# Optimization experiments

Hardware: AMD Instinct MI355X
Metric: run time of the kernel (lower is better)

Reference implementation:

```python
import jax, jax.numpy as jnp
import numpy as np

TOP_K = 2


def setup_inputs() -> dict:
    key = jax.random.key(0)
    k1, k2, k3, k4, k5 = jax.random.split(key, 5)
    B, S, D, E, F = 2, 1024, 2048, 8, 768
    scale_in = 1.0 / np.sqrt(D)
    scale_ff = 1.0 / np.sqrt(F)
    return {
        "x": jax.random.normal(k1, (B, S, D), dtype=jnp.float32),
        "w_gate_router": jax.random.normal(k2, (E, D), dtype=jnp.float32) * scale_in,
        "w_gate_proj": jax.random.normal(k3, (E, F, D), dtype=jnp.float32) * scale_in,
        "w_up_proj": jax.random.normal(k4, (E, F, D), dtype=jnp.float32) * scale_in,
        "w_down_proj": jax.random.normal(k5, (E, D, F), dtype=jnp.float32) * scale_ff,
    }


def moe_forward(x, w_gate_router, w_gate_proj, w_up_proj, w_down_proj):
    E = w_gate_router.shape[0]
    # Router: scores [B,S,E], top-k selection, softmax over the k selected scores.
    scores = jnp.einsum("bsd,ed->bse", x, w_gate_router)
    topk_scores, topk_idx = jax.lax.top_k(scores, TOP_K)          # [B,S,K]
    topk_probs = jax.nn.softmax(topk_scores, axis=-1)             # [B,S,K]
    # Dense combine weights: zero for unselected experts (== scatter of topk_probs).
    weights = jnp.sum(topk_probs[..., None] * jax.nn.one_hot(topk_idx, E, dtype=x.dtype), axis=-2)  # [B,S,E]
    # Per-expert SwiGLU computed densely over all tokens (same math as
    # gather/dispatch-per-expert followed by scatter-add combine).
    gate = jnp.einsum("bsd,efd->bsef", x, w_gate_proj)            # [B,S,E,F]
    up = jnp.einsum("bsd,efd->bsef", x, w_up_proj)
    hidden = jax.nn.silu(gate) * up                                # [B,S,E,F]
    # Weighted combine: sum_e weights[b,s,e] * (hidden @ w_down[e].T)
    out = jnp.einsum("bsef,edf,bse->bsd", hidden, w_down_proj, weights)
    return out


def reference(x, w_gate_router, w_gate_proj, w_up_proj, w_down_proj):
    return moe_forward(x, w_gate_router, w_gate_proj, w_up_proj, w_down_proj)
```

## Files before the change

### kernel.cpp

```cpp
#include <hip/hip_runtime.h>

#define T_TOK 2048
#define DIM   2048
#define NEXP  8
#define FF    768
#define NGRP  16

typedef unsigned short u16;
typedef unsigned int   u32;
typedef __bf16 bf16x8 __attribute__((ext_vector_type(8)));
typedef float  f32x4  __attribute__((ext_vector_type(4)));
typedef u16    u16x4  __attribute__((ext_vector_type(4)));

#define AS1 __attribute__((address_space(1)))
#define AS3 __attribute__((address_space(3)))

__device__ __forceinline__ u16 f2bf(float f) {
    union { u32 i; float f; } v; v.f = f;
    u32 r = v.i + 0x7FFF + ((v.i >> 16) & 1);
    return (u16)(r >> 16);
}

__device__ __forceinline__ void gload16(const u16* g, u16* l) {
    __builtin_amdgcn_global_load_lds((const AS1 u32*)g, (AS3 u32*)l, 16, 0, 0);
}

__global__ void cvt_kernel(const float* __restrict__ s, u16* __restrict__ d, int n4) {
    int i = blockIdx.x * blockDim.x + threadIdx.x;
    int st = gridDim.x * blockDim.x;
    for (; i < n4; i += st) {
        f32x4 v = ((const f32x4*)s)[i];
        u16x4 o;
#pragma unroll
        for (int j = 0; j < 4; j++) o[j] = f2bf(v[j]);
        ((u16x4*)d)[i] = o;
    }
}

__global__ void router_kernel(const float* __restrict__ x, const float* __restrict__ wr,
                              int* cnt, int* rt_e, float* rt_p) {
    int t = blockIdx.x;
    int lane = threadIdx.x;
    float xv[32];
#pragma unroll
    for (int i = 0; i < 32; i++) xv[i] = x[(size_t)t * DIM + i * 64 + lane];
    float s[NEXP];
#pragma unroll
    for (int e = 0; e < NEXP; e++) {
        float acc = 0.f;
#pragma unroll
        for (int i = 0; i < 32; i++) acc += xv[i] * wr[(size_t)e * DIM + i * 64 + lane];
        for (int off = 32; off; off >>= 1) acc += __shfl_xor(acc, off);
        s[e] = acc;
    }
    if (lane == 0) {
        int bi = 0; float bv = s[0];
        for (int e = 1; e < NEXP; e++) if (s[e] > bv) { bv = s[e]; bi = e; }
        float sv = -1e30f; int si = 0;
        for (int e = 0; e < NEXP; e++) { if (e == bi) continue; if (s[e] > sv) { sv = s[e]; si = e; } }
        float p0 = 1.f / (1.f + __expf(sv - bv));
        float p1 = 1.f - p0;
        rt_e[t * 2 + 0] = bi; rt_e[t * 2 + 1] = si;
        rt_p[t * 2 + 0] = p0; rt_p[t * 2 + 1] = p1;
        atomicAdd(&cnt[bi * 2 + 0], 1);
        atomicAdd(&cnt[si * 2 + 1], 1);
    }
}

__global__ void scan_kernel(const int* cnt, int* base, int* tile_g, int* tile_m0, int* ntiles) {
    if (threadIdx.x == 0 && blockIdx.x == 0) {
        int off = 0, nt = 0;
        for (int g = 0; g < NGRP; g++) {
            base[g] = off;
            int c = cnt[g];
            for (int m0 = 0; m0 < c; m0 += 128) { tile_g[nt] = g; tile_m0[nt] = m0; nt++; }
            off += c;
        }
        *ntiles = nt;
    }
}

__global__ void assign_kernel(const int* rt_e, const float* rt_p, const int* base,
                              int* poscnt, int* rowtok, float* rowprob) {
    int t = blockIdx.x * blockDim.x + threadIdx.x;
    if (t >= T_TOK) return;
    for (int k = 0; k < 2; k++) {
        int g = rt_e[t * 2 + k] * 2 + k;
        int pos = atomicAdd(&poscnt[g], 1);
        int row = base[g] + pos;
        rowtok[row] = t;
        rowprob[row] = rt_p[t * 2 + k];
    }
}

__launch_bounds__(256)
__global__ void gateup_kernel(const u16* __restrict__ xb, const u16* __restrict__ wgb,
                              const u16* __restrict__ wub,
                              const int* cnt, const int* base, const int* tile_g,
                              const int* tile_m0, const int* ntiles,
                              const int* rowtok, const float* rowprob,
                              u16* __restrict__ hidden) {
    int tile = blockIdx.x;
    if (tile >= *ntiles) return;
    int g = tile_g[tile], m0 = tile_m0[tile];
    int e = g >> 1;
    int f0 = blockIdx.y * 64;
    int cg = cnt[g], bg_ = base[g];

    __shared__ u16 As[128 * 32];
    __shared__ u16 Bs[128 * 32];
    __shared__ int   tks[128];
    __shared__ float ps[128];

    int tid = threadIdx.x;
    if (tid < 128) {
        int valid = (m0 + tid) < cg;
        tks[tid] = valid ? rowtok[bg_ + m0 + tid] : 0;
        ps[tid]  = valid ? rowprob[bg_ + m0 + tid] : 0.f;
    }
    __syncthreads();

    int wave = tid >> 6, lane = tid & 63;
    int quad = lane >> 4, l16 = lane & 15;
    int wr = wave >> 1, wc = wave & 1;

    int r4   = lane >> 2;
    int koff = (lane & 3) * 8;
    int arow0 = wave * 32 + r4;
    const u16* ga0 = xb + (size_t)tks[arow0] * DIM + koff;
    const u16* ga1 = xb + (size_t)tks[arow0 + 16] * DIM + koff;
    int c0 = wave * 2;
    const u16* wsrc0 = (c0 & 1) ? wub : wgb;
    const u16* wsrc1 = ((c0 + 1) & 1) ? wub : wgb;
    const u16* gb0 = wsrc0 + ((size_t)e * FF + f0 + ((c0) >> 1) * 16 + r4) * DIM + koff;
    const u16* gb1 = wsrc1 + ((size_t)e * FF + f0 + ((c0 + 1) >> 1) * 16 + r4) * DIM + koff;
    u16* lA0 = &As[(wave * 32) * 32];
    u16* lA1 = &As[(wave * 32 + 16) * 32];
    u16* lB0 = &Bs[(c0 * 16) * 32];
    u16* lB1 = &Bs[((c0 + 1) * 16) * 32];

    f32x4 acc[4][4] = {};

    for (int kk = 0; kk < DIM; kk += 32) {
        gload16(ga0 + kk, lA0);
        gload16(ga1 + kk, lA1);
        gload16(gb0 + kk, lB0);
        gload16(gb1 + kk, lB1);
        __syncthreads();
        bf16x8 a[4], b[4];
#pragma unroll
        for (int mi = 0; mi < 4; mi++)
            a[mi] = *(const bf16x8*)&As[(wr * 64 + mi * 16 + l16) * 32 + quad * 8];
#pragma unroll
        for (int ni = 0; ni < 4; ni++)
            b[ni] = *(const bf16x8*)&Bs[(wc * 64 + ni * 16 + l16) * 32 + quad * 8];
#pragma unroll
        for (int mi = 0; mi < 4; mi++)
#pragma unroll
            for (int ni = 0; ni < 4; ni++)
                acc[mi][ni] = __builtin_amdgcn_mfma_f32_16x16x32_bf16(a[mi], b[ni], acc[mi][ni], 0, 0, 0);
        __syncthreads();
    }

#pragma unroll
    for (int mi = 0; mi < 4; mi++) {
#pragma unroll
        for (int p = 0; p < 2; p++) {
            int f = f0 + (wc * 2 + p) * 16 + l16;
#pragma unroll
            for (int r = 0; r < 4; r++) {
                int m = wr * 64 + mi * 16 + quad * 4 + r;
                if (m0 + m < cg) {
                    float gv = acc[mi][p * 2][r], uv = acc[mi][p * 2 + 1][r];
                    float h = (gv / (1.f + __expf(-gv))) * uv * ps[m];
                    hidden[(size_t)(bg_ + m0 + m) * FF + f] = f2bf(h);
                }
            }
        }
    }
}

__launch_bounds__(256)
__global__ void down_kernel(const u16* __restrict__ hid, const u16* __restrict__ wdb,
                            const int* cnt, const int* base, const int* tile_g,
                            const int* tile_m0, const int* ntiles, const int* rowtok,
                            float* __restrict__ out) {
    int tile = blockIdx.x;
    if (tile >= *ntiles) return;
    int g = tile_g[tile], m0 = tile_m0[tile];
    int e = g >> 1;
    int d0 = blockIdx.y * 128;
    int cg = cnt[g], bg_ = base[g];

    __shared__ u16 As[128 * 32];
    __shared__ u16 Bs[128 * 32];
    __shared__ int tks[128];

    int tid = threadIdx.x;
    if (tid < 128) tks[tid] = ((m0 + tid) < cg) ? rowtok[bg_ + m0 + tid] : 0;
    __syncthreads();

    int wave = tid >> 6, lane = tid & 63;
    int quad = lane >> 4, l16 = lane & 15;
    int wr = wave >> 1, wc = wave & 1;

    int r4   = lane >> 2;
    int koff = (lane & 3) * 8;
    int arow0 = wave * 32 + r4;
    const u16* ga0 = hid + (size_t)(bg_ + m0 + arow0) * FF + koff;
    const u16* ga1 = hid + (size_t)(bg_ + m0 + arow0 + 16) * FF + koff;
    int c0 = wave * 2;
    const u16* gb0 = wdb + ((size_t)e * DIM + d0 + c0 * 16 + r4) * FF + koff;
    const u16* gb1 = wdb + ((size_t)e * DIM + d0 + (c0 + 1) * 16 + r4) * FF + koff;
    u16* lA0 = &As[(wave * 32) * 32];
    u16* lA1 = &As[(wave * 32 + 16) * 32];
    u16* lB0 = &Bs[(c0 * 16) * 32];
    u16* lB1 = &Bs[((c0 + 1) * 16) * 32];

    f32x4 acc[4][4] = {};

    for (int kk = 0; kk < FF; kk += 32) {
        gload16(ga0 + kk, lA0);
        gload16(ga1 + kk, lA1);
        gload16(gb0 + kk, lB0);
        gload16(gb1 + kk, lB1);
        __syncthreads();
        bf16x8 a[4], b[4];
#pragma unroll
        for (int mi = 0; mi < 4; mi++)
            a[mi] = *(const bf16x8*)&As[(wr * 64 + mi * 16 + l16) * 32 + quad * 8];
#pragma unroll
        for (int ni = 0; ni < 4; ni++)
            b[ni] = *(const bf16x8*)&Bs[(wc * 64 + ni * 16 + l16) * 32 + quad * 8];
#pragma unroll
        for (int mi = 0; mi < 4; mi++)
#pragma unroll
            for (int ni = 0; ni < 4; ni++)
                acc[mi][ni] = __builtin_amdgcn_mfma_f32_16x16x32_bf16(a[mi], b[ni], acc[mi][ni], 0, 0, 0);
        __syncthreads();
    }

#pragma unroll
    for (int mi = 0; mi < 4; mi++) {
#pragma unroll
        for (int ni = 0; ni < 4; ni++) {
            int d = d0 + wc * 64 + ni * 16 + l16;
#pragma unroll
            for (int r = 0; r < 4; r++) {
                int m = wr * 64 + mi * 16 + quad * 4 + r;
                if (m0 + m < cg) {
                    atomicAdd(&out[(size_t)tks[m] * DIM + d], acc[mi][ni][r]);
                }
            }
        }
    }
}

extern "C" void kernel_launch(void* const* d_in, const int* in_sizes, int n_in,
                              void* d_out, int out_size, void* d_ws, size_t ws_size,
                              hipStream_t stream) {
    const float* x  = (const float*)d_in[0];
    const float* wr = (const float*)d_in[1];
    const float* wg = (const float*)d_in[2];
    const float* wu = (const float*)d_in[3];
    const float* wd = (const float*)d_in[4];
    float* out = (float*)d_out;

    char* W = (char*)d_ws;
    int*   cnt     = (int*)(W + 0);
    int*   poscnt  = (int*)(W + 64);
    int*   base    = (int*)(W + 128);
    int*   ntiles  = (int*)(W + 192);
    int*   tile_g  = (int*)(W + 256);
    int*   tile_m0 = (int*)(W + 512);
    int*   rt_e    = (int*)(W + 1024);
    float* rt_p    = (float*)(W + 20480);
    int*   rowtok  = (int*)(W + 40960);
    float* rowprob = (float*)(W + 61440);
    u16*   hidden  = (u16*)(W + 81920);
    u16*   xb      = (u16*)(W + ((size_t)8  << 20));
    u16*   wgb     = (u16*)(W + ((size_t)17 << 20));
    u16*   wub     = (u16*)(W + ((size_t)43 << 20));
    u16*   wdb     = (u16*)(W + ((size_t)69 << 20));

    hipMemsetAsync(W, 0, 256, stream);
    hipMemsetAsync(d_out, 0, (size_t)out_size * 4, stream);

    const int NW = NEXP * FF * DIM / 4;
    const int NX = T_TOK * DIM / 4;
    cvt_kernel<<<1280, 256, 0, stream>>>(x,  xb,  NX);
    cvt_kernel<<<1280, 256, 0, stream>>>(wg, wgb, NW);
    cvt_kernel<<<1280, 256, 0, stream>>>(wu, wub, NW);
    cvt_kernel<<<1280, 256, 0, stream>>>(wd, wdb, NW);

    router_kernel<<<T_TOK, 64, 0, stream>>>(x, wr, cnt, rt_e, rt_p);
    scan_kernel<<<1, 64, 0, stream>>>(cnt, base, tile_g, tile_m0, ntiles);
    assign_kernel<<<8, 256, 0, stream>>>(rt_e, rt_p, base, poscnt, rowtok, rowprob);

    gateup_kernel<<<dim3(48, 12), 256, 0, stream>>>(xb, wgb, wub, cnt, base, tile_g, tile_m0,
                                                    ntiles, rowtok, rowprob, hidden);
    down_kernel<<<dim3(48, 16), 256, 0, stream>>>(hidden, wdb, cnt, base, tile_g, tile_m0,
                                                  ntiles, rowtok, out);
}
```

Baseline: 394.0 us.

## Merge weight conversions, double K-tile depth, replace atomics with per-slot bf16 combine

The four fp32-to-bf16 conversion launches become one kernel indexed by grid y. Both GEMM kernels now load 64-wide K tiles into LDS, halving the number of barrier pairs per K sweep. The down projection stops doing fp32 atomicAdd into a zeroed output: each top-k slot writes its own bf16 buffer, reusing the wgb region after gate/up finishes, and a final combine kernel adds the two buffers into fp32. This drops the output memset and the atomic traffic, but rounds partial results to bf16 and assumes each token appears exactly once per slot.

```diff
diff --git a/kernel.cpp b/kernel.cpp
--- a/kernel.cpp
+++ b/kernel.cpp
@@ -11,6 +11,7 @@
 typedef __bf16 bf16x8 __attribute__((ext_vector_type(8)));
 typedef float  f32x4  __attribute__((ext_vector_type(4)));
 typedef u16    u16x4  __attribute__((ext_vector_type(4)));
+typedef u16    u16x8  __attribute__((ext_vector_type(8)));
 
 #define AS1 __attribute__((address_space(1)))
 #define AS3 __attribute__((address_space(3)))
@@ -20,12 +21,25 @@
     u32 r = v.i + 0x7FFF + ((v.i >> 16) & 1);
     return (u16)(r >> 16);
 }
+__device__ __forceinline__ float bf2f(u16 u) {
+    union { u32 i; float f; } v; v.i = ((u32)u) << 16; return v.f;
+}
 
 __device__ __forceinline__ void gload16(const u16* g, u16* l) {
     __builtin_amdgcn_global_load_lds((const AS1 u32*)g, (AS3 u32*)l, 16, 0, 0);
 }
 
-__global__ void cvt_kernel(const float* __restrict__ s, u16* __restrict__ d, int n4) {
+__global__ void cvt4_kernel(const float* __restrict__ s0, u16* __restrict__ d0, int n0,
+                            const float* __restrict__ s1, u16* __restrict__ d1, int n1,
+                            const float* __restrict__ s2, u16* __restrict__ d2, int n2,
+                            const float* __restrict__ s3, u16* __restrict__ d3, int n3) {
+    const float* s; u16* d; int n4;
+    switch (blockIdx.y) {
+        case 0: s = s0; d = d0; n4 = n0; break;
+        case 1: s = s1; d = d1; n4 = n1; break;
+        case 2: s = s2; d = d2; n4 = n2; break;
+        default: s = s3; d = d3; n4 = n3; break;
+    }
     int i = blockIdx.x * blockDim.x + threadIdx.x;
     int st = gridDim.x * blockDim.x;
     for (; i < n4; i += st) {
@@ -107,8 +121,8 @@
     int f0 = blockIdx.y * 64;
     int cg = cnt[g], bg_ = base[g];
 
-    __shared__ u16 As[128 * 32];
-    __shared__ u16 Bs[128 * 32];
+    __shared__ u16 As[128 * 64];
+    __shared__ u16 Bs[128 * 64];
     __shared__ int   tks[128];
     __shared__ float ps[128];
 
@@ -124,41 +138,45 @@
     int quad = lane >> 4, l16 = lane & 15;
     int wr = wave >> 1, wc = wave & 1;
 
-    int r4   = lane >> 2;
-    int koff = (lane & 3) * 8;
-    int arow0 = wave * 32 + r4;
-    const u16* ga0 = xb + (size_t)tks[arow0] * DIM + koff;
-    const u16* ga1 = xb + (size_t)tks[arow0 + 16] * DIM + koff;
-    int c0 = wave * 2;
-    const u16* wsrc0 = (c0 & 1) ? wub : wgb;
-    const u16* wsrc1 = ((c0 + 1) & 1) ? wub : wgb;
-    const u16* gb0 = wsrc0 + ((size_t)e * FF + f0 + ((c0) >> 1) * 16 + r4) * DIM + koff;
-    const u16* gb1 = wsrc1 + ((size_t)e * FF + f0 + ((c0 + 1) >> 1) * 16 + r4) * DIM + koff;
-    u16* lA0 = &As[(wave * 32) * 32];
-    u16* lA1 = &As[(wave * 32 + 16) * 32];
-    u16* lB0 = &Bs[(c0 * 16) * 32];
-    u16* lB1 = &Bs[((c0 + 1) * 16) * 32];
+    int r8   = lane >> 3;
+    int koff = (lane & 7) * 8;
+    const u16* ga[4]; const u16* gb[4];
+    u16 *lA[4], *lB[4];
+#pragma unroll
+    for (int j = 0; j < 4; j++) {
+        int arow = wave * 32 + j * 8 + r8;
+        ga[j] = xb + (size_t)tks[arow] * DIM + koff;
+        lA[j] = &As[(wave * 32 + j * 8) * 64];
+        int c = wave * 2 + (j >> 1);
+        const u16* src = (c & 1) ? wub : wgb;
+        gb[j] = src + ((size_t)e * FF + f0 + (c >> 1) * 16 + (j & 1) * 8 + r8) * DIM + koff;
+        lB[j] = &Bs[(wave * 32 + j * 8) * 64];
+    }
 
     f32x4 acc[4][4] = {};
 
-    for (int kk = 0; kk < DIM; kk += 32) {
-        gload16(ga0 + kk, lA0);
-        gload16(ga1 + kk, lA1);
-        gload16(gb0 + kk, lB0);
-        gload16(gb1 + kk, lB1);
+    for (int kk = 0; kk < DIM; kk += 64) {
+#pragma unroll
+        for (int j = 0; j < 4; j++) {
+            gload16(ga[j] + kk, lA[j]);
+            gload16(gb[j] + kk, lB[j]);
+        }
         __syncthreads();
-        bf16x8 a[4], b[4];
-#pragma unroll
-        for (int mi = 0; mi < 4; mi++)
-            a[mi] = *(const bf16x8*)&As[(wr * 64 + mi * 16 + l16) * 32 + quad * 8];
-#pragma unroll
-        for (int ni = 0; ni < 4; ni++)
-            b[ni] = *(const bf16x8*)&Bs[(wc * 64 + ni * 16 + l16) * 32 + quad * 8];
-#pragma unroll
-        for (int mi = 0; mi < 4; mi++)
+#pragma unroll
+        for (int ks = 0; ks < 2; ks++) {
+            bf16x8 a[4], b[4];
+#pragma unroll
+            for (int mi = 0; mi < 4; mi++)
+                a[mi] = *(const bf16x8*)&As[(wr * 64 + mi * 16 + l16) * 64 + ks * 32 + quad * 8];
 #pragma unroll
             for (int ni = 0; ni < 4; ni++)
-                acc[mi][ni] = __builtin_amdgcn_mfma_f32_16x16x32_bf16(a[mi], b[ni], acc[mi][ni], 0, 0, 0);
+                b[ni] = *(const bf16x8*)&Bs[(wc * 64 + ni * 16 + l16) * 64 + ks * 32 + quad * 8];
+#pragma unroll
+            for (int mi = 0; mi < 4; mi++)
+#pragma unroll
+                for (int ni = 0; ni < 4; ni++)
+                    acc[mi][ni] = __builtin_amdgcn_mfma_f32_16x16x32_bf16(a[mi], b[ni], acc[mi][ni], 0, 0, 0);
+        }
         __syncthreads();
     }
 
@@ -184,16 +202,16 @@
 __global__ void down_kernel(const u16* __restrict__ hid, const u16* __restrict__ wdb,
                             const int* cnt, const int* base, const int* tile_g,
                             const int* tile_m0, const int* ntiles, const int* rowtok,
-                            float* __restrict__ out) {
+                            u16* __restrict__ out0, u16* __restrict__ out1) {
     int tile = blockIdx.x;
     if (tile >= *ntiles) return;
     int g = tile_g[tile], m0 = tile_m0[tile];
-    int e = g >> 1;
+    int e = g >> 1, slot = g & 1;
     int d0 = blockIdx.y * 128;
     int cg = cnt[g], bg_ = base[g];
 
-    __shared__ u16 As[128 * 32];
-    __shared__ u16 Bs[128 * 32];
+    __shared__ u16 As[128 * 64];
+    __shared__ u16 Bs[128 * 64];
     __shared__ int tks[128];
 
     int tid = threadIdx.x;
@@ -204,42 +222,46 @@
     int quad = lane >> 4, l16 = lane & 15;
     int wr = wave >> 1, wc = wave & 1;
 
-    int r4   = lane >> 2;
-    int koff = (lane & 3) * 8;
-    int arow0 = wave * 32 + r4;
-    const u16* ga0 = hid + (size_t)(bg_ + m0 + arow0) * FF + koff;
-    const u16* ga1 = hid + (size_t)(bg_ + m0 + arow0 + 16) * FF + koff;
-    int c0 = wave * 2;
-    const u16* gb0 = wdb + ((size_t)e * DIM + d0 + c0 * 16 + r4) * FF + koff;
-    const u16* gb1 = wdb + ((size_t)e * DIM + d0 + (c0 + 1) * 16 + r4) * FF + koff;
-    u16* lA0 = &As[(wave * 32) * 32];
-    u16* lA1 = &As[(wave * 32 + 16) * 32];
-    u16* lB0 = &Bs[(c0 * 16) * 32];
-    u16* lB1 = &Bs[((c0 + 1) * 16) * 32];
+    int r8   = lane >> 3;
+    int koff = (lane & 7) * 8;
+    const u16* ga[4]; const u16* gb[4];
+    u16 *lA[4], *lB[4];
+#pragma unroll
+    for (int j = 0; j < 4; j++) {
+        ga[j] = hid + (size_t)(bg_ + m0 + wave * 32 + j * 8 + r8) * FF + koff;
+        lA[j] = &As[(wave * 32 + j * 8) * 64];
+        gb[j] = wdb + ((size_t)e * DIM + d0 + wave * 32 + j * 8 + r8) * FF + koff;
+        lB[j] = &Bs[(wave * 32 + j * 8) * 64];
+    }
 
     f32x4 acc[4][4] = {};
 
-    for (int kk = 0; kk < FF; kk += 32) {
-        gload16(ga0 + kk, lA0);
-        gload16(ga1 + kk, lA1);
-        gload16(gb0 + kk, lB0);
-        gload16(gb1 + kk, lB1);
+    for (int kk = 0; kk < FF; kk += 64) {
+#pragma unroll
+        for (int j = 0; j < 4; j++) {
+            gload16(ga[j] + kk, lA[j]);
+            gload16(gb[j] + kk, lB[j]);
+        }
         __syncthreads();
-        bf16x8 a[4], b[4];
-#pragma unroll
-        for (int mi = 0; mi < 4; mi++)
-            a[mi] = *(const bf16x8*)&As[(wr * 64 + mi * 16 + l16) * 32 + quad * 8];
-#pragma unroll
-        for (int ni = 0; ni < 4; ni++)
-            b[ni] = *(const bf16x8*)&Bs[(wc * 64 + ni * 16 + l16) * 32 + quad * 8];
-#pragma unroll
-        for (int mi = 0; mi < 4; mi++)
+#pragma unroll
+        for (int ks = 0; ks < 2; ks++) {
+            bf16x8 a[4], b[4];
+#pragma unroll
+            for (int mi = 0; mi < 4; mi++)
+                a[mi] = *(const bf16x8*)&As[(wr * 64 + mi * 16 + l16) * 64 + ks * 32 + quad * 8];
 #pragma unroll
             for (int ni = 0; ni < 4; ni++)
-                acc[mi][ni] = __builtin_amdgcn_mfma_f32_16x16x32_bf16(a[mi], b[ni], acc[mi][ni], 0, 0, 0);
+                b[ni] = *(const bf16x8*)&Bs[(wc * 64 + ni * 16 + l16) * 64 + ks * 32 + quad * 8];
+#pragma unroll
+            for (int mi = 0; mi < 4; mi++)
+#pragma unroll
+                for (int ni = 0; ni < 4; ni++)
+                    acc[mi][ni] = __builtin_amdgcn_mfma_f32_16x16x32_bf16(a[mi], b[ni], acc[mi][ni], 0, 0, 0);
+        }
         __syncthreads();
     }
 
+    u16* outp = slot ? out1 : out0;
 #pragma unroll
     for (int mi = 0; mi < 4; mi++) {
 #pragma unroll
@@ -249,11 +271,26 @@
             for (int r = 0; r < 4; r++) {
                 int m = wr * 64 + mi * 16 + quad * 4 + r;
                 if (m0 + m < cg) {
-                    atomicAdd(&out[(size_t)tks[m] * DIM + d], acc[mi][ni][r]);
+                    outp[(size_t)tks[m] * DIM + d] = f2bf(acc[mi][ni][r]);
                 }
             }
         }
     }
+}
+
+__global__ void combine_kernel(const u16* __restrict__ o0, const u16* __restrict__ o1,
+                               float* __restrict__ out) {
+    int i = blockIdx.x * blockDim.x + threadIdx.x;
+    u16x8 a = *(const u16x8*)(o0 + (size_t)i * 8);
+    u16x8 b = *(const u16x8*)(o1 + (size_t)i * 8);
+    f32x4 r0, r1;
+#pragma unroll
+    for (int j = 0; j < 4; j++) {
+        r0[j] = bf2f(a[j]) + bf2f(b[j]);
+        r1[j] = bf2f(a[4 + j]) + bf2f(b[4 + j]);
+    }
+    *(f32x4*)(out + (size_t)i * 8) = r0;
+    *(f32x4*)(out + (size_t)i * 8 + 4) = r1;
 }
 
 extern "C" void kernel_launch(void* const* d_in, const int* in_sizes, int n_in,
@@ -282,16 +319,14 @@
     u16*   wgb     = (u16*)(W + ((size_t)17 << 20));
     u16*   wub     = (u16*)(W + ((size_t)43 << 20));
     u16*   wdb     = (u16*)(W + ((size_t)69 << 20));
+    u16*   out0    = (u16*)(W + ((size_t)17 << 20));
+    u16*   out1    = (u16*)(W + ((size_t)26 << 20));
 
     hipMemsetAsync(W, 0, 256, stream);
-    hipMemsetAsync(d_out, 0, (size_t)out_size * 4, stream);
 
     const int NW = NEXP * FF * DIM / 4;
     const int NX = T_TOK * DIM / 4;
-    cvt_kernel<<<1280, 256, 0, stream>>>(x,  xb,  NX);
-    cvt_kernel<<<1280, 256, 0, stream>>>(wg, wgb, NW);
-    cvt_kernel<<<1280, 256, 0, stream>>>(wu, wub, NW);
-    cvt_kernel<<<1280, 256, 0, stream>>>(wd, wdb, NW);
+    cvt4_kernel<<<dim3(1536, 4), 256, 0, stream>>>(x, xb, NX, wg, wgb, NW, wu, wub, NW, wd, wdb, NW);
 
     router_kernel<<<T_TOK, 64, 0, stream>>>(x, wr, cnt, rt_e, rt_p);
     scan_kernel<<<1, 64, 0, stream>>>(cnt, base, tile_g, tile_m0, ntiles);
@@ -300,5 +335,6 @@
     gateup_kernel<<<dim3(48, 12), 256, 0, stream>>>(xb, wgb, wub, cnt, base, tile_g, tile_m0,
                                                     ntiles, rowtok, rowprob, hidden);
     down_kernel<<<dim3(48, 16), 256, 0, stream>>>(hidden, wdb, cnt, base, tile_g, tile_m0,
-                                                  ntiles, rowtok, out);
-}
+                                                  ntiles, rowtok, out0, out1);
+    combine_kernel<<<T_TOK * DIM / (256 * 8), 256, 0, stream>>>(out0, out1, out);
+}
```

After: 412.4 us. 1.05x slower.
